# Performance work log

Hardware: AMD Instinct MI355X
Metric: run time of the kernel (lower is better)

The kernel has to match this reference:

```python
import jax, jax.numpy as jnp
import numpy as np

BETA = 0.25


def setup_inputs() -> dict:
    key = jax.random.key(0)
    k1, k2 = jax.random.split(key)
    z_e = jax.random.normal(k1, (16, 64, 64, 64), dtype=jnp.float32)  # (B, D, H, W)
    embedding = jax.random.normal(k2, (1024, 64), dtype=jnp.float32)  # (K, D)
    return {"z_e": z_e, "embedding": embedding}


def reference(z_e, embedding):
    B, D, H, W = z_e.shape
    # (B, D, H, W) -> (B, H, W, D) -> (N, D)
    flat = jnp.transpose(z_e, (0, 2, 3, 1)).reshape(-1, D)
    # squared L2 distances to codebook: (N, K)
    dist = (jnp.sum(flat * flat, axis=1, keepdims=True)
            + jnp.sum(embedding * embedding, axis=1)
            - 2.0 * flat @ embedding.T)
    indices = jnp.argmin(dist, axis=1)  # (N,)
    z_q_flat = embedding[indices]  # (N, D) gather
    z_q = jnp.transpose(z_q_flat.reshape(B, H, W, D), (0, 3, 1, 2))  # (B, D, H, W)
    codebook_loss = jnp.mean((jax.lax.stop_gradient(z_q) - z_e) ** 2)
    commit_loss = jnp.mean((z_q - jax.lax.stop_gradient(z_e)) ** 2)
    vq_loss = codebook_loss + BETA * commit_loss
    # straight-through estimator
    z_q_st = z_e + jax.lax.stop_gradient(z_q - z_e)
    return (z_q_st, vq_loss, indices.reshape(B, H, W))
```

## Files before the change

### kernel.cpp

```cpp
#include <hip/hip_runtime.h>
#include <math.h>

typedef short  short8 __attribute__((ext_vector_type(8)));
typedef float  f32x4  __attribute__((ext_vector_type(4)));

#define ZQ_ELEMS 4194304
#define KC       1024
#define EPS_HALF 0.005f


__device__ inline unsigned short bf16_rne(float f) {
    union { float fv; unsigned u; } a; a.fv = f;
    unsigned r = a.u + 0x7FFFu + ((a.u >> 16) & 1u);
    return (unsigned short)(r >> 16);
}
__device__ inline float bf16_to_f(unsigned short h) {
    union { unsigned u; float fv; } a; a.u = ((unsigned)h) << 16;
    return a.fv;
}
__device__ inline double dpack(float hi, unsigned lo) {
    return __hiloint2double(__float_as_int(hi), (int)lo);
}
__device__ inline float dhi(double d) { return __int_as_float(__double2hiint(d)); }
__device__ inline unsigned dlo(double d) { return (unsigned)__double2loint(d); }

__global__ __launch_bounds__(256) void vq_prep(const float* __restrict__ emb,
        unsigned short* __restrict__ epack, float* __restrict__ enorm,
        int* __restrict__ risky_cnt, float* __restrict__ out) {
    const int k = blockIdx.x * 256 + threadIdx.x;
    if (k == 0) { *risky_cnt = 0; out[ZQ_ELEMS] = 0.f; }
    const float4* e4 = (const float4*)(emb + k * 64);
    float s = 0.f;
#pragma unroll
    for (int j = 0; j < 16; ++j) {
        float4 v = e4[j];
        float vv[4] = {v.x, v.y, v.z, v.w};
        ushort4 hv, lv;
        unsigned short h[4], l[4];
#pragma unroll
        for (int t = 0; t < 4; ++t) {
            s = fmaf(vv[t], vv[t], s);
            h[t] = bf16_rne(vv[t]);
            l[t] = bf16_rne(vv[t] - bf16_to_f(h[t]));
        }
        hv.x = h[0]; hv.y = h[1]; hv.z = h[2]; hv.w = h[3];
        lv.x = l[0]; lv.y = l[1]; lv.z = l[2]; lv.w = l[3];
        *(ushort4*)(epack + k * 128 + j * 4)      = hv;
        *(ushort4*)(epack + k * 128 + 64 + j * 4) = lv;
    }
    enorm[k] = s;
}

__global__ __launch_bounds__(256) void vq_scan(const float* __restrict__ z_e,
        const unsigned short* __restrict__ epack, const float* __restrict__ enorm,
        const float* __restrict__ emb, float* __restrict__ out,
        int* __restrict__ risky_cnt, int* __restrict__ risky) {
    const int tid  = threadIdx.x;
    const int lane = tid & 63;
    const int col  = lane & 15;
    const int g    = lane >> 4;
    const int wv   = __builtin_amdgcn_readfirstlane(tid >> 6);
    const int pblk = blockIdx.x * 64;

    __shared__ __align__(16) char smem[19456];
    unsigned short* afrag = (unsigned short*)smem;
    double* mrgB = (double*)(smem + 16384);
    float*  mrgS = (float*)(smem + 18432);
    float (*zq)[65] = (float (*)[65])smem;
    __shared__ int   sidx[64];
    __shared__ float sred[4];

    {
        const int lp = tid & 63;
        const int pg = pblk + lp;
        const float* zb = z_e + (pg >> 12) * 262144 + (pg & 4095);
        const int sx = (lp & 7) << 3;
#pragma unroll
        for (int s8 = 0; s8 < 2; ++s8) {
            const int d0 = wv * 16 + s8 * 8;
            short8 H, L;
#pragma unroll
            for (int j = 0; j < 8; ++j) {
                float v = zb[(d0 + j) * 4096];
                unsigned short h = bf16_rne(v);
                H[j] = (short)h;
                L[j] = (short)bf16_rne(v - bf16_to_f(h));
            }
            const int sw = d0 ^ sx;
            *(short8*)&afrag[lp * 128 + sw]      = H;
            *(short8*)&afrag[lp * 128 + 64 + sw] = L;
        }
    }
    __syncthreads();

    const f32x4 zero4 = {0.f, 0.f, 0.f, 0.f};
    const int g8 = g * 8;

    double Brun[4];
    float  Srun[4];
#pragma unroll
    for (int it = 0; it < 4; ++it) { Brun[it] = dpack(-INFINITY, 0u); Srun[it] = -INFINITY; }

#pragma unroll 1
    for (int pass = 0; pass < 4; ++pass) {
        const int cbase = pass * 256 + wv * 64;
        short8 ah[4][2], al[4][2];
        f32x4 enf[4];
#pragma unroll
        for (int t = 0; t < 4; ++t) {
            const int code = cbase + t * 16 + col;
            const short8* ph = (const short8*)(epack + code * 128) + g;
            ah[t][0] = ph[0]; ah[t][1] = ph[4];
            al[t][0] = ph[8]; al[t][1] = ph[12];
            const float4 e4 = *(const float4*)(enorm + cbase + t * 16 + g * 4);
            enf[t][0] = -0.5f * e4.x; enf[t][1] = -0.5f * e4.y;
            enf[t][2] = -0.5f * e4.z; enf[t][3] = -0.5f * e4.w;
        }
        const int K1 = 1023 - cbase - g * 4;

#pragma unroll
        for (int it = 0; it < 4; ++it) {
            const int lpx = it * 16 + col;
            const int sxp = (lpx & 7) << 3;
            const unsigned short* ap = &afrag[lpx * 128];
            const short8 bh0 = *(const short8*)&ap[(g8     ) ^ sxp];
            const short8 bh1 = *(const short8*)&ap[(32 + g8) ^ sxp];
            const short8 bl0 = *(const short8*)&ap[64 + ((g8     ) ^ sxp)];
            const short8 bl1 = *(const short8*)&ap[64 + ((32 + g8) ^ sxp)];

            double B = Brun[it];
            float  S = Srun[it];
#pragma unroll
            for (int t = 0; t < 4; ++t) {
                f32x4 aA, aB;
                aA = __builtin_amdgcn_mfma_f32_16x16x32_bf16(ah[t][0], bh0, enf[t], 0, 0, 0);
                aB = __builtin_amdgcn_mfma_f32_16x16x32_bf16(ah[t][1], bh1, zero4, 0, 0, 0);
                aA = __builtin_amdgcn_mfma_f32_16x16x32_bf16(al[t][0], bh0, aA, 0, 0, 0);
                aB = __builtin_amdgcn_mfma_f32_16x16x32_bf16(al[t][1], bh1, aB, 0, 0, 0);
                aA = __builtin_amdgcn_mfma_f32_16x16x32_bf16(ah[t][0], bl0, aA, 0, 0, 0);
                aB = __builtin_amdgcn_mfma_f32_16x16x32_bf16(ah[t][1], bl1, aB, 0, 0, 0);
#pragma unroll
                for (int r = 0; r < 4; ++r) {
                    const float v = aA[r] + aB[r];
                    S = __builtin_amdgcn_fmed3f(dhi(B), S, v);
                    B = fmax(B, dpack(v, (unsigned)(K1 - t * 16 - r)));
                }
            }
            Brun[it] = B;
            Srun[it] = S;
        }
    }

#pragma unroll
    for (int it = 0; it < 4; ++it) {
        double B = Brun[it];
        float  S = Srun[it];
#pragma unroll
        for (int s = 16; s < 64; s <<= 1) {
            const double ob = __shfl_xor(B, s, 64);
            const float  o2 = __shfl_xor(S, s, 64);
            S = __builtin_amdgcn_fmed3f(dhi(B), dhi(ob), fmaxf(S, o2));
            B = fmax(B, ob);
        }
        Brun[it] = B;
        Srun[it] = S;
    }
    __syncthreads();
    if (g == 0) {
#pragma unroll
        for (int it = 0; it < 4; ++it) {
            mrgB[wv * 64 + it * 16 + col] = Brun[it];
            mrgS[wv * 64 + it * 16 + col] = Srun[it];
        }
    }
    __syncthreads();

    if (tid < 64) {
        double B = mrgB[tid];
        float  S = mrgS[tid];
#pragma unroll
        for (int w = 1; w < 4; ++w) {
            const double ob = mrgB[w * 64 + tid];
            const float  o2 = mrgS[w * 64 + tid];
            S = __builtin_amdgcn_fmed3f(dhi(B), dhi(ob), fmaxf(S, o2));
            B = fmax(B, ob);
        }
        const int idx = 1023 - (int)dlo(B);
        sidx[tid] = idx;
        out[ZQ_ELEMS + 1 + pblk + tid] = (float)idx;
        const bool risk = (dhi(B) - S < EPS_HALF);
        const unsigned long long m = __ballot(risk);
        int base = 0;
        if (lane == 0 && m) base = atomicAdd(risky_cnt, __popcll(m));
        base = __shfl(base, 0, 64);
        if (risk) risky[base + __popcll(m & ((1ull << lane) - 1ull))] = pblk + tid;
    }
    __syncthreads();

#pragma unroll
    for (int i = 0; i < 16; ++i) {
        const int p = wv * 16 + i;
        const int k = sidx[p];
        zq[p][lane] = emb[k * 64 + lane];
    }
    __syncthreads();

    const int batch = pblk >> 12;
    const int hw0   = pblk & 4095;
    const int p4 = (tid & 15) * 4;
    const float* zeb = z_e + batch * 262144 + hw0;
    float* ob = out + batch * 262144 + hw0;
    float ss = 0.f;
#pragma unroll
    for (int it = 0; it < 4; ++it) {
        const int d = (tid >> 4) + it * 16;
        float4 q;
        q.x = zq[p4 + 0][d]; q.y = zq[p4 + 1][d];
        q.z = zq[p4 + 2][d]; q.w = zq[p4 + 3][d];
        const float4 z = *(const float4*)(zeb + d * 4096 + p4);
        *(float4*)(ob + d * 4096 + p4) = q;
        const float e0 = q.x - z.x, e1 = q.y - z.y, e2 = q.z - z.z, e3 = q.w - z.w;
        ss += e0 * e0 + e1 * e1 + e2 * e2 + e3 * e3;
    }
    for (int off = 32; off; off >>= 1) ss += __shfl_down(ss, off, 64);
    if (lane == 0) sred[wv] = ss;
    __syncthreads();
    if (tid == 0)
        atomicAdd(out + ZQ_ELEMS,
                  ((sred[0] + sred[1]) + (sred[2] + sred[3])) * (1.25f / (float)ZQ_ELEMS));
}

__global__ __launch_bounds__(256) void vq_fix(const float* __restrict__ z_e,
        const float* __restrict__ emb, float* __restrict__ out,
        const int* __restrict__ cnt, const int* __restrict__ list) {
    const int n = *cnt;
    if ((int)blockIdx.x * 4 >= n) return;
    __shared__ float etile[64][65];
    const int tid  = threadIdx.x;
    const int lane = tid & 63;
    const int wv   = __builtin_amdgcn_readfirstlane(tid >> 6);

    for (int base = blockIdx.x * 4; base < n; base += gridDim.x * 4) {
        const int item = base + wv;
        const bool active = item < n;
        int pix = 0, oldk = 0;
        float f[64];
        if (active) {
            pix = list[item];
            const float* zb = z_e + (pix >> 12) * 262144 + (pix & 4095);
#pragma unroll
            for (int d = 0; d < 64; ++d) f[d] = zb[d * 4096];
            oldk = (int)out[ZQ_ELEMS + 1 + pix];
        }
        double best = INFINITY; int bk = KC;
        double dold = 0.0;
        for (int j = 0; j < 16; ++j) {
            __syncthreads();
#pragma unroll
            for (int i = 0; i < 16; ++i) {
                const int idx = i * 256 + tid;
                etile[idx >> 6][idx & 63] = emb[j * 4096 + idx];
            }
            __syncthreads();
            if (active) {
                const int k = j * 64 + lane;
                double a0 = 0.0, a1 = 0.0;
#pragma unroll
                for (int d = 0; d < 64; d += 2) {
                    const double d0 = (double)f[d]     - (double)etile[lane][d];
                    const double d1 = (double)f[d + 1] - (double)etile[lane][d + 1];
                    a0 = fma(d0, d0, a0);
                    a1 = fma(d1, d1, a1);
                }
                const double acc = a0 + a1;
                if (acc < best || (acc == best && k < bk)) { best = acc; bk = k; }
                if (k == oldk) dold = acc;
            }
        }
        if (active) {
            for (int off = 32; off; off >>= 1) {
                const double ov = __shfl_down(best, off, 64);
                const int    oi = __shfl_down(bk, off, 64);
                if (ov < best || (ov == best && oi < bk)) { best = ov; bk = oi; }
            }
            for (int off = 32; off; off >>= 1) dold += __shfl_down(dold, off, 64);
            bk   = __shfl(bk, 0, 64);
            best = __shfl(best, 0, 64);
            dold = __shfl(dold, 0, 64);
            if (bk != oldk) {
                if (lane == 0) out[ZQ_ELEMS + 1 + pix] = (float)bk;
                out[(pix >> 12) * 262144 + (pix & 4095) + lane * 4096] = emb[bk * 64 + lane];
                if (lane == 0)
                    atomicAdd(out + ZQ_ELEMS,
                              (float)((best - dold) * (1.25 / (double)ZQ_ELEMS)));
            }
        }
    }
}

extern "C" void kernel_launch(void* const* d_in, const int* in_sizes, int n_in,
                              void* d_out, int out_size, void* d_ws, size_t ws_size,
                              hipStream_t stream) {
    const float* z_e = (const float*)d_in[0];
    const float* emb = (const float*)d_in[1];
    float* out = (float*)d_out;
    char* ws = (char*)d_ws;
    unsigned short* epack = (unsigned short*)ws;
    float*  enorm     = (float*)(ws + 262144);
    int*    risky_cnt = (int*)(ws + 266240);
    int*    risky     = (int*)(ws + 270336);

    vq_prep<<<4, 256, 0, stream>>>(emb, epack, enorm, risky_cnt, out);
    vq_scan<<<1024, 256, 0, stream>>>(z_e, epack, enorm, emb, out, risky_cnt, risky);
    vq_fix<<<512, 256, 0, stream>>>(z_e, emb, out, risky_cnt, risky);
}
```

Baseline: 78.71 us.

## Tree-reduce argmin candidates in scan and batch four pixels per wave in fix

```diff
diff --git a/kernel.cpp b/kernel.cpp
--- a/kernel.cpp
+++ b/kernel.cpp
@@ -128,8 +128,7 @@
             const short8 bl0 = *(const short8*)&ap[64 + ((g8     ) ^ sxp)];
             const short8 bl1 = *(const short8*)&ap[64 + ((32 + g8) ^ sxp)];
 
-            double B = Brun[it];
-            float  S = Srun[it];
+            double cand[16];
 #pragma unroll
             for (int t = 0; t < 4; ++t) {
                 f32x4 aA, aB;
@@ -140,14 +139,27 @@
                 aA = __builtin_amdgcn_mfma_f32_16x16x32_bf16(ah[t][0], bl0, aA, 0, 0, 0);
                 aB = __builtin_amdgcn_mfma_f32_16x16x32_bf16(ah[t][1], bl1, aB, 0, 0, 0);
 #pragma unroll
-                for (int r = 0; r < 4; ++r) {
-                    const float v = aA[r] + aB[r];
-                    S = __builtin_amdgcn_fmed3f(dhi(B), S, v);
-                    B = fmax(B, dpack(v, (unsigned)(K1 - t * 16 - r)));
+                for (int r = 0; r < 4; ++r)
+                    cand[t * 4 + r] = dpack(aA[r] + aB[r], (unsigned)(K1 - t * 16 - r));
+            }
+            double tB[8]; float tS[8];
+#pragma unroll
+            for (int i = 0; i < 8; ++i) {
+                tB[i] = fmax(cand[2 * i], cand[2 * i + 1]);
+                tS[i] = fminf(dhi(cand[2 * i]), dhi(cand[2 * i + 1]));
+            }
+#pragma unroll
+            for (int lvl = 4; lvl >= 1; lvl >>= 1) {
+#pragma unroll
+                for (int i = 0; i < lvl; ++i) {
+                    tS[i] = __builtin_amdgcn_fmed3f(dhi(tB[i]), dhi(tB[i + lvl]),
+                                                    fmaxf(tS[i], tS[i + lvl]));
+                    tB[i] = fmax(tB[i], tB[i + lvl]);
                 }
             }
-            Brun[it] = B;
-            Srun[it] = S;
+            Srun[it] = __builtin_amdgcn_fmed3f(dhi(Brun[it]), dhi(tB[0]),
+                                               fmaxf(Srun[it], tS[0]));
+            Brun[it] = fmax(Brun[it], tB[0]);
         }
     }
 
@@ -234,26 +246,31 @@
         const float* __restrict__ emb, float* __restrict__ out,
         const int* __restrict__ cnt, const int* __restrict__ list) {
     const int n = *cnt;
-    if ((int)blockIdx.x * 4 >= n) return;
+    if ((int)blockIdx.x * 16 >= n) return;
     __shared__ float etile[64][65];
     const int tid  = threadIdx.x;
     const int lane = tid & 63;
     const int wv   = __builtin_amdgcn_readfirstlane(tid >> 6);
 
-    for (int base = blockIdx.x * 4; base < n; base += gridDim.x * 4) {
-        const int item = base + wv;
-        const bool active = item < n;
-        int pix = 0, oldk = 0;
-        float f[64];
-        if (active) {
-            pix = list[item];
-            const float* zb = z_e + (pix >> 12) * 262144 + (pix & 4095);
-#pragma unroll
-            for (int d = 0; d < 64; ++d) f[d] = zb[d * 4096];
-            oldk = (int)out[ZQ_ELEMS + 1 + pix];
-        }
-        double best = INFINITY; int bk = KC;
-        double dold = 0.0;
+    for (int base = blockIdx.x * 16; base < n; base += gridDim.x * 16) {
+        int   pix[4], oldk[4];
+        bool  act[4];
+        float f[4][64];
+        double best[4]; int bk[4]; double dold[4];
+#pragma unroll
+        for (int q = 0; q < 4; ++q) {
+            const int item = base + q * 4 + wv;
+            act[q] = item < n;
+            pix[q] = 0; oldk[q] = 0;
+            best[q] = INFINITY; bk[q] = KC; dold[q] = 0.0;
+            if (act[q]) {
+                pix[q] = list[item];
+                const float* zb = z_e + (pix[q] >> 12) * 262144 + (pix[q] & 4095);
+#pragma unroll
+                for (int d = 0; d < 64; ++d) f[q][d] = zb[d * 4096];
+                oldk[q] = (int)out[ZQ_ELEMS + 1 + pix[q]];
+            }
+        }
         for (int j = 0; j < 16; ++j) {
             __syncthreads();
 #pragma unroll
@@ -262,37 +279,43 @@
                 etile[idx >> 6][idx & 63] = emb[j * 4096 + idx];
             }
             __syncthreads();
-            if (active) {
-                const int k = j * 64 + lane;
+            const int k = j * 64 + lane;
+#pragma unroll
+            for (int q = 0; q < 4; ++q) {
+                if (!act[q]) continue;
                 double a0 = 0.0, a1 = 0.0;
 #pragma unroll
                 for (int d = 0; d < 64; d += 2) {
-                    const double d0 = (double)f[d]     - (double)etile[lane][d];
-                    const double d1 = (double)f[d + 1] - (double)etile[lane][d + 1];
+                    const double d0 = (double)f[q][d]     - (double)etile[lane][d];
+                    const double d1 = (double)f[q][d + 1] - (double)etile[lane][d + 1];
                     a0 = fma(d0, d0, a0);
                     a1 = fma(d1, d1, a1);
                 }
                 const double acc = a0 + a1;
-                if (acc < best || (acc == best && k < bk)) { best = acc; bk = k; }
-                if (k == oldk) dold = acc;
-            }
-        }
-        if (active) {
+                if (acc < best[q] || (acc == best[q] && k < bk[q])) { best[q] = acc; bk[q] = k; }
+                if (k == oldk[q]) dold[q] = acc;
+            }
+        }
+#pragma unroll
+        for (int q = 0; q < 4; ++q) {
+            if (!act[q]) continue;
+            double b = best[q]; int i1 = bk[q]; double dd = dold[q];
             for (int off = 32; off; off >>= 1) {
-                const double ov = __shfl_down(best, off, 64);
-                const int    oi = __shfl_down(bk, off, 64);
-                if (ov < best || (ov == best && oi < bk)) { best = ov; bk = oi; }
-            }
-            for (int off = 32; off; off >>= 1) dold += __shfl_down(dold, off, 64);
-            bk   = __shfl(bk, 0, 64);
-            best = __shfl(best, 0, 64);
-            dold = __shfl(dold, 0, 64);
-            if (bk != oldk) {
-                if (lane == 0) out[ZQ_ELEMS + 1 + pix] = (float)bk;
-                out[(pix >> 12) * 262144 + (pix & 4095) + lane * 4096] = emb[bk * 64 + lane];
+                const double ov = __shfl_down(b, off, 64);
+                const int    oi = __shfl_down(i1, off, 64);
+                if (ov < b || (ov == b && oi < i1)) { b = ov; i1 = oi; }
+            }
+            for (int off = 32; off; off >>= 1) dd += __shfl_down(dd, off, 64);
+            i1 = __shfl(i1, 0, 64);
+            b  = __shfl(b, 0, 64);
+            dd = __shfl(dd, 0, 64);
+            if (i1 != oldk[q]) {
+                if (lane == 0) out[ZQ_ELEMS + 1 + pix[q]] = (float)i1;
+                out[(pix[q] >> 12) * 262144 + (pix[q] & 4095) + lane * 4096] =
+                    emb[i1 * 64 + lane];
                 if (lane == 0)
                     atomicAdd(out + ZQ_ELEMS,
-                              (float)((best - dold) * (1.25 / (double)ZQ_ELEMS)));
+                              (float)((b - dd) * (1.25 / (double)ZQ_ELEMS)));
             }
         }
     }
@@ -312,5 +335,5 @@
 
     vq_prep<<<4, 256, 0, stream>>>(emb, epack, enorm, risky_cnt, out);
     vq_scan<<<1024, 256, 0, stream>>>(z_e, epack, enorm, emb, out, risky_cnt, risky);
-    vq_fix<<<512, 256, 0, stream>>>(z_e, emb, out, risky_cnt, risky);
-}
+    vq_fix<<<128, 256, 0, stream>>>(z_e, emb, out, risky_cnt, risky);
+}
```

New measurement: 222.6 us. +182.8%, slower.
